# Kernel optimization log

Measured on AMD Instinct MI355X. Metric: run time of the kernel, lower is better.

Reference implementation:

```python
import jax, jax.numpy as jnp
import numpy as np

B, N, D = 64, 4096, 512
ATT = 128


def setup_inputs() -> dict:
    key = jax.random.key(0)
    ks = jax.random.split(key, 7)
    s = lambda fan_in: 1.0 / np.sqrt(fan_in)
    return {
        "v_I": jax.random.normal(ks[0], (B, N, D), dtype=jnp.float32),
        "v_Q": jax.random.normal(ks[1], (B, D), dtype=jnp.float32),
        "W_I": jax.random.normal(ks[2], (D, ATT), dtype=jnp.float32) * s(D),
        "W_Q": jax.random.normal(ks[3], (D, ATT), dtype=jnp.float32) * s(D),
        "b_Q": jnp.zeros((ATT,), dtype=jnp.float32),
        "W_p": jax.random.normal(ks[4], (ATT, 1), dtype=jnp.float32) * s(ATT),
        "b_p": jnp.zeros((1,), dtype=jnp.float32),
    }


def reference(v_I, v_Q, W_I, W_Q, b_Q, W_p, b_p):
    # v_I: [B, N, D], v_Q: [B, D]
    v_I_att = jnp.tanh(jnp.einsum("bnd,da->bna", v_I, W_I))          # [B, N, A]
    v_Q_att = jnp.tanh(v_Q @ W_Q + b_Q)[:, None, :]                  # [B, 1, A]
    h_A = jnp.tanh(v_I_att + v_Q_att)                                # [B, N, A]
    # dropout is identity in inference/reference mode
    p_I = (jnp.einsum("bna,ao->bno", h_A, W_p) + b_p)[..., 0]        # [B, N]
    p_I_output = jax.nn.softmax(p_I, axis=-1)                        # [B, N]
    v_att = jnp.einsum("bn,bnd->bd", p_I_output, v_I)                # [B, D]
    u = v_att + v_Q                                                  # [B, D]
    return (p_I_output, u)
```

## Files before the change

kernel.cpp:

```cpp
#include <hip/hip_runtime.h>
#include <cstdint>
#include <cstddef>

#define B_ 64
#define N_ 4096
#define D_ 512
#define A_ 128

typedef unsigned short u16;
typedef __attribute__((ext_vector_type(8))) short bf16x8;
typedef __attribute__((ext_vector_type(4))) float f32x4;

__device__ __forceinline__ u16 cvt_bf16(float x) {
    unsigned u = __float_as_uint(x);
    return (u16)((u + 0x7FFFu + ((u >> 16) & 1u)) >> 16);
}
__device__ __forceinline__ unsigned pack2_bf16(float a, float b) {
    unsigned ua = __float_as_uint(a), ub = __float_as_uint(b);
    unsigned ra = (ua + 0x7FFFu + ((ua >> 16) & 1u)) >> 16;
    unsigned rb = (ub + 0x7FFFu + ((ub >> 16) & 1u)) >> 16;
    return ra | (rb << 16);
}
__device__ __forceinline__ float bf2f(unsigned lo16) {
    return __uint_as_float(lo16 << 16);
}
__device__ __forceinline__ float fast_tanh(float x) {
    float ax = fabsf(x);
    float e  = __expf(-2.0f * ax);
    float r  = __fdividef(1.0f - e, 1.0f + e);
    return x < 0.0f ? -r : r;
}

#define WAITVM(N) asm volatile("s_waitcnt vmcnt(" #N ")" ::: "memory")
#define SCHEDB()  __builtin_amdgcn_sched_barrier(0)

__global__ void k_prep(const float* __restrict__ WI, const float* __restrict__ vQ,
                       const float* __restrict__ WQ, const float* __restrict__ bQ,
                       u16* __restrict__ Wbf, float* __restrict__ qatt,
                       float* __restrict__ sums, float* __restrict__ u_raw) {
    const int blk = blockIdx.x, t = threadIdx.x;
    if (blk < 64) {
        #pragma unroll
        for (int i = 0; i < 2; ++i) {
            int item = blk * 256 + i * 128 + t;
            int a  = item & 127;
            int d0 = (item >> 7) << 2;
            ushort4 r;
            r.x = cvt_bf16(WI[(d0 + 0) * A_ + a]);
            r.y = cvt_bf16(WI[(d0 + 1) * A_ + a]);
            r.z = cvt_bf16(WI[(d0 + 2) * A_ + a]);
            r.w = cvt_bf16(WI[(d0 + 3) * A_ + a]);
            int off = (a >> 4) * 8192
                    + (d0 >> 5) * 512
                    + ((d0 >> 3) & 3) * 128
                    + (a & 15) * 8
                    + (d0 & 7);
            *(ushort4*)&Wbf[off] = r;
        }
    } else {
        const int b = blk - 64;
        __shared__ float sq[D_];
        for (int d = t; d < D_; d += 128) sq[d] = vQ[b * D_ + d];
        __syncthreads();
        float acc = bQ[t];
        #pragma unroll 8
        for (int d = 0; d < D_; ++d) acc += sq[d] * WQ[d * A_ + t];
        qatt[b * A_ + t] = fast_tanh(acc);
        float4 z = {0.f, 0.f, 0.f, 0.f};
        *(float4*)(u_raw + b * D_ + t * 4) = z;
        if (t == 0) sums[b] = 0.0f;
    }
}

__global__ void __launch_bounds__(512, 4)
k_fused(const float* __restrict__ vI, const u16* __restrict__ Wbf,
        const float* __restrict__ qatt, const float* __restrict__ Wp,
        float* __restrict__ wbuf, float* __restrict__ sums,
        float* __restrict__ u_raw) {
    const int b  = blockIdx.y;
    const int n0 = blockIdx.x * 64;
    const int t    = threadIdx.x;
    const int lane = t & 63, wave = t >> 6;
    const int l15  = lane & 15, quad = lane >> 4;
    const int rg = wave >> 1, cg = wave & 1;

    __shared__ u16   sA[64 * 512];
    __shared__ float sred[2][64];
    __shared__ float sw[64];
    __shared__ float sph[4][512];

    float qa[4], wp[4];
    #pragma unroll
    for (int nt = 0; nt < 4; ++nt) {
        int a = (cg * 4 + nt) * 16 + l15;
        qa[nt] = qatt[b * A_ + a];
        wp[nt] = Wp[a];
    }
    SCHEDB();

    const int ar = t >> 3;
    const int ak = (t & 7) * 8;
    const float* ag = vI + ((size_t)(b * N_ + n0 + ar) * D_ + ak);
    char* awb = (char*)sA + ar * 1024 + (((t & 7) * 16) ^ ((ar & 7) << 4));

    const u16* bg = Wbf + lane * 8;

    const int arow = rg * 16 + l15;
    const char* afb = (const char*)sA + arow * 1024;
    const int aswz = (arow & 7) << 4;

    f32x4 acc[4];
    #pragma unroll
    for (int i = 0; i < 4; ++i) acc[i] = (f32x4){0.f, 0.f, 0.f, 0.f};

    float4 areg[2][2];
    areg[0][0] = *(const float4*)(ag + 0);
    areg[0][1] = *(const float4*)(ag + 4);
    SCHEDB();

    bf16x8 bf0[4], bf1[4];

    #pragma unroll
    for (int kr = 0; kr < 8; ++kr) {
        #pragma unroll
        for (int nt = 0; nt < 4; ++nt)
            bf0[nt] = *(const bf16x8*)(bg + ((((cg * 4 + nt) * 16) + kr * 2 + 0) << 9));
        SCHEDB();
        #pragma unroll
        for (int nt = 0; nt < 4; ++nt)
            bf1[nt] = *(const bf16x8*)(bg + ((((cg * 4 + nt) * 16) + kr * 2 + 1) << 9));
        SCHEDB();
        if (kr < 7) {
            areg[(kr + 1) & 1][0] = *(const float4*)(ag + (kr + 1) * 64);
            areg[(kr + 1) & 1][1] = *(const float4*)(ag + (kr + 1) * 64 + 4);
        }
        SCHEDB();

        if (kr < 7) { WAITVM(10); } else { WAITVM(8); }
        {
            float4 x0 = areg[kr & 1][0], x1 = areg[kr & 1][1];
            union { bf16x8 v; unsigned u[4]; } cv;
            cv.u[0] = pack2_bf16(x0.x, x0.y);
            cv.u[1] = pack2_bf16(x0.z, x0.w);
            cv.u[2] = pack2_bf16(x1.x, x1.y);
            cv.u[3] = pack2_bf16(x1.z, x1.w);
            *(bf16x8*)(awb + kr * 128) = cv.v;
        }
        SCHEDB();
        asm volatile("s_waitcnt lgkmcnt(0)" ::: "memory");
        __builtin_amdgcn_s_barrier();
        SCHEDB();

        if (kr < 7) { WAITVM(6); } else { WAITVM(4); }
        {
            bf16x8 af = *(const bf16x8*)(afb + kr * 128 + ((quad * 16) ^ aswz));
            #pragma unroll
            for (int nt = 0; nt < 4; ++nt)
                acc[nt] = __builtin_amdgcn_mfma_f32_16x16x32_bf16(af, bf0[nt], acc[nt], 0, 0, 0);
        }
        SCHEDB();
        if (kr < 7) { WAITVM(2); } else { WAITVM(0); }
        {
            bf16x8 af = *(const bf16x8*)(afb + kr * 128 + ((64 + quad * 16) ^ aswz));
            #pragma unroll
            for (int nt = 0; nt < 4; ++nt)
                acc[nt] = __builtin_amdgcn_mfma_f32_16x16x32_bf16(af, bf1[nt], acc[nt], 0, 0, 0);
        }
        SCHEDB();
    }

    #pragma unroll
    for (int r = 0; r < 4; ++r) {
        float s = 0.f;
        #pragma unroll
        for (int nt = 0; nt < 4; ++nt) {
            float t1 = fast_tanh(acc[nt][r]);
            float h  = fast_tanh(t1 + qa[nt]);
            s += h * wp[nt];
        }
        s += __shfl_xor(s, 1, 16);
        s += __shfl_xor(s, 2, 16);
        s += __shfl_xor(s, 4, 16);
        s += __shfl_xor(s, 8, 16);
        if (l15 == 0) sred[cg][rg * 16 + quad * 4 + r] = s;
    }
    __syncthreads();
    if (t < 64) {
        float we = __expf(sred[0][t] + sred[1][t]);
        sw[t] = we;
        wbuf[(size_t)b * N_ + n0 + t] = we;
        float ls = we;
        ls += __shfl_xor(ls, 1);
        ls += __shfl_xor(ls, 2);
        ls += __shfl_xor(ls, 4);
        ls += __shfl_xor(ls, 8);
        ls += __shfl_xor(ls, 16);
        ls += __shfl_xor(ls, 32);
        if (t == 0) atomicAdd(sums + b, ls);
    }
    __syncthreads();

    const int dg = t & 127;
    const int rr = t >> 7;
    float p0 = 0.f, p1 = 0.f, p2 = 0.f, p3 = 0.f;
    #pragma unroll
    for (int i = 0; i < 16; ++i) {
        int n = i * 4 + rr;
        const char* src = (const char*)sA + n * 1024 + ((dg * 8) ^ ((n & 7) << 4));
        uint2 wv = *(const uint2*)src;
        float wn = sw[n];
        p0 += wn * bf2f(wv.x & 0xffffu);
        p1 += wn * bf2f(wv.x >> 16);
        p2 += wn * bf2f(wv.y & 0xffffu);
        p3 += wn * bf2f(wv.y >> 16);
    }
    *(float4*)&sph[rr][dg * 4] = (float4){p0, p1, p2, p3};
    __syncthreads();
    {
        int d = t;
        float v = sph[0][d] + sph[1][d] + sph[2][d] + sph[3][d];
        atomicAdd(u_raw + (size_t)b * D_ + d, v);
    }
}

__global__ void __launch_bounds__(256)
k_fin(const float* __restrict__ wbuf, const float* __restrict__ sums,
      const float* __restrict__ u_raw, const float* __restrict__ vQ,
      float* __restrict__ p_out, float* __restrict__ u_out) {
    const int b = blockIdx.x, t = threadIdx.x;
    const float inv = 1.0f / sums[b];
    #pragma unroll
    for (int i = 0; i < 4; ++i) {
        float4 x = *(const float4*)(wbuf + (size_t)b * N_ + i * 1024 + t * 4);
        float4 y = { x.x * inv, x.y * inv, x.z * inv, x.w * inv };
        *(float4*)(p_out + (size_t)b * N_ + i * 1024 + t * 4) = y;
    }
    if (t < 128) {
        float4 ur = *(const float4*)(u_raw + b * D_ + t * 4);
        float4 vq = *(const float4*)(vQ + b * D_ + t * 4);
        float4 o  = { ur.x * inv + vq.x, ur.y * inv + vq.y,
                      ur.z * inv + vq.z, ur.w * inv + vq.w };
        *(float4*)(u_out + b * D_ + t * 4) = o;
    }
}

extern "C" void kernel_launch(void* const* d_in, const int* in_sizes, int n_in,
                              void* d_out, int out_size, void* d_ws, size_t ws_size,
                              hipStream_t stream) {
    const float* vI = (const float*)d_in[0];
    const float* vQ = (const float*)d_in[1];
    const float* WI = (const float*)d_in[2];
    const float* WQ = (const float*)d_in[3];
    const float* bQ = (const float*)d_in[4];
    const float* Wp = (const float*)d_in[5];

    float* out_p = (float*)d_out;
    float* out_u = out_p + (size_t)B_ * N_;

    char* ws = (char*)d_ws;
    u16*   Wbf   = (u16*)ws;
    float* qatt  = (float*)(ws + 131072);
    float* sums  = (float*)(ws + 163840);
    float* u_raw = (float*)(ws + 164864);
    float* wbuf  = (float*)(ws + 295936);

    k_prep<<<128, 128, 0, stream>>>(WI, vQ, WQ, bQ, Wbf, qatt, sums, u_raw);
    k_fused<<<dim3(N_ / 64, B_), 512, 0, stream>>>(vI, Wbf, qatt, Wp,
                                                   wbuf, sums, u_raw);
    k_fin<<<B_, 256, 0, stream>>>(wbuf, sums, u_raw, vQ, out_p, out_u);
}
```

Before: 762.6 us.

## Stage W_I tiles into LDS via global_load_lds shared across waves

Each wave previously loaded its own bf16 weight fragments straight from global memory into registers, so waves sharing a column group fetched the same data twice. Each wave now copies one 16-row slice of the weight tile into LDS per k-step with direct global-to-LDS loads, and all waves read B fragments from LDS. This adds a second barrier per iteration and raises LDS use to 80 KB, which may limit blocks per CU. The MFMA section also runs at raised wave priority, and the finalize kernel is split across four blocks per batch row to add parallelism.

```diff
diff --git a/kernel.cpp b/kernel.cpp
--- a/kernel.cpp
+++ b/kernel.cpp
@@ -29,6 +29,11 @@
     float e  = __expf(-2.0f * ax);
     float r  = __fdividef(1.0f - e, 1.0f + e);
     return x < 0.0f ? -r : r;
+}
+__device__ __forceinline__ void gl_lds16(const void* g, void* l) {
+    __builtin_amdgcn_global_load_lds(
+        (const __attribute__((address_space(1))) unsigned int*)g,
+        (__attribute__((address_space(3))) unsigned int*)l, 16, 0, 0);
 }
 
 #define WAITVM(N) asm volatile("s_waitcnt vmcnt(" #N ")" ::: "memory")
@@ -84,10 +89,12 @@
     const int l15  = lane & 15, quad = lane >> 4;
     const int rg = wave >> 1, cg = wave & 1;
 
-    __shared__ u16   sA[64 * 512];
-    __shared__ float sred[2][64];
-    __shared__ float sw[64];
-    __shared__ float sph[4][512];
+    __shared__ __align__(16) char smem[81920];
+    u16*  sA = (u16*)smem;
+    char* sB = smem + 65536;
+    float* sph  = (float*)sB;
+    float* sw   = (float*)(sB + 8192);
+    float* sred = (float*)(sB + 8448);
 
     float qa[4], wp[4];
     #pragma unroll
@@ -98,16 +105,18 @@
     }
     SCHEDB();
 
-    const int ar = t >> 3;
-    const int ak = (t & 7) * 8;
-    const float* ag = vI + ((size_t)(b * N_ + n0 + ar) * D_ + ak);
-    char* awb = (char*)sA + ar * 1024 + (((t & 7) * 16) ^ ((ar & 7) << 4));
-
-    const u16* bg = Wbf + lane * 8;
+    const int ar  = t >> 3;
+    const int akx = t & 7;
+    const float* ag = vI + ((size_t)(b * N_ + n0 + ar) * D_ + akx * 8);
+    char* awb = (char*)sA + ar * 1024 + ((akx * 16) ^ ((ar & 7) << 4));
+
+    const u16* bsrc = Wbf + (size_t)(wave * 16) * 512 + lane * 8;
+    char* bdst = sB + wave * 2048;
 
     const int arow = rg * 16 + l15;
     const char* afb = (const char*)sA + arow * 1024;
     const int aswz = (arow & 7) << 4;
+    const char* bfb = sB + (cg * 4) * 2048 + lane * 16;
 
     f32x4 acc[4];
     #pragma unroll
@@ -116,27 +125,20 @@
     float4 areg[2][2];
     areg[0][0] = *(const float4*)(ag + 0);
     areg[0][1] = *(const float4*)(ag + 4);
+    WAITVM(2);
     SCHEDB();
 
-    bf16x8 bf0[4], bf1[4];
-
     #pragma unroll
     for (int kr = 0; kr < 8; ++kr) {
-        #pragma unroll
-        for (int nt = 0; nt < 4; ++nt)
-            bf0[nt] = *(const bf16x8*)(bg + ((((cg * 4 + nt) * 16) + kr * 2 + 0) << 9));
-        SCHEDB();
-        #pragma unroll
-        for (int nt = 0; nt < 4; ++nt)
-            bf1[nt] = *(const bf16x8*)(bg + ((((cg * 4 + nt) * 16) + kr * 2 + 1) << 9));
+        gl_lds16(bsrc + (kr * 2 + 0) * 512, bdst);
+        gl_lds16(bsrc + (kr * 2 + 1) * 512, bdst + 1024);
         SCHEDB();
         if (kr < 7) {
             areg[(kr + 1) & 1][0] = *(const float4*)(ag + (kr + 1) * 64);
             areg[(kr + 1) & 1][1] = *(const float4*)(ag + (kr + 1) * 64 + 4);
         }
         SCHEDB();
-
-        if (kr < 7) { WAITVM(10); } else { WAITVM(8); }
+        if (kr < 7) { WAITVM(4); } else { WAITVM(2); }
         {
             float4 x0 = areg[kr & 1][0], x1 = areg[kr & 1][1];
             union { bf16x8 v; unsigned u[4]; } cv;
@@ -147,25 +149,23 @@
             *(bf16x8*)(awb + kr * 128) = cv.v;
         }
         SCHEDB();
+        if (kr < 7) { WAITVM(2); } else { WAITVM(0); }
         asm volatile("s_waitcnt lgkmcnt(0)" ::: "memory");
         __builtin_amdgcn_s_barrier();
         SCHEDB();
-
-        if (kr < 7) { WAITVM(6); } else { WAITVM(4); }
-        {
-            bf16x8 af = *(const bf16x8*)(afb + kr * 128 + ((quad * 16) ^ aswz));
+        __builtin_amdgcn_s_setprio(1);
+        #pragma unroll
+        for (int ks = 0; ks < 2; ++ks) {
+            bf16x8 af = *(const bf16x8*)(afb + kr * 128 + ((ks * 64 + quad * 16) ^ aswz));
             #pragma unroll
-            for (int nt = 0; nt < 4; ++nt)
-                acc[nt] = __builtin_amdgcn_mfma_f32_16x16x32_bf16(af, bf0[nt], acc[nt], 0, 0, 0);
-        }
-        SCHEDB();
-        if (kr < 7) { WAITVM(2); } else { WAITVM(0); }
-        {
-            bf16x8 af = *(const bf16x8*)(afb + kr * 128 + ((64 + quad * 16) ^ aswz));
-            #pragma unroll
-            for (int nt = 0; nt < 4; ++nt)
-                acc[nt] = __builtin_amdgcn_mfma_f32_16x16x32_bf16(af, bf1[nt], acc[nt], 0, 0, 0);
-        }
+            for (int nt = 0; nt < 4; ++nt) {
+                bf16x8 bv = *(const bf16x8*)(bfb + nt * 2048 + ks * 1024);
+                acc[nt] = __builtin_amdgcn_mfma_f32_16x16x32_bf16(af, bv, acc[nt], 0, 0, 0);
+            }
+        }
+        __builtin_amdgcn_s_setprio(0);
+        SCHEDB();
+        __builtin_amdgcn_s_barrier();
         SCHEDB();
     }
 
@@ -182,11 +182,11 @@
         s += __shfl_xor(s, 2, 16);
         s += __shfl_xor(s, 4, 16);
         s += __shfl_xor(s, 8, 16);
-        if (l15 == 0) sred[cg][rg * 16 + quad * 4 + r] = s;
+        if (l15 == 0) sred[cg * 64 + rg * 16 + quad * 4 + r] = s;
     }
     __syncthreads();
     if (t < 64) {
-        float we = __expf(sred[0][t] + sred[1][t]);
+        float we = __expf(sred[t] + sred[64 + t]);
         sw[t] = we;
         wbuf[(size_t)b * N_ + n0 + t] = we;
         float ls = we;
@@ -214,11 +214,11 @@
         p2 += wn * bf2f(wv.y & 0xffffu);
         p3 += wn * bf2f(wv.y >> 16);
     }
-    *(float4*)&sph[rr][dg * 4] = (float4){p0, p1, p2, p3};
+    *(float4*)(sph + rr * 512 + dg * 4) = (float4){p0, p1, p2, p3};
     __syncthreads();
     {
         int d = t;
-        float v = sph[0][d] + sph[1][d] + sph[2][d] + sph[3][d];
+        float v = sph[d] + sph[512 + d] + sph[1024 + d] + sph[1536 + d];
         atomicAdd(u_raw + (size_t)b * D_ + d, v);
     }
 }
@@ -227,15 +227,15 @@
 k_fin(const float* __restrict__ wbuf, const float* __restrict__ sums,
       const float* __restrict__ u_raw, const float* __restrict__ vQ,
       float* __restrict__ p_out, float* __restrict__ u_out) {
-    const int b = blockIdx.x, t = threadIdx.x;
+    const int b = blockIdx.x, q = blockIdx.y, t = threadIdx.x;
     const float inv = 1.0f / sums[b];
-    #pragma unroll
-    for (int i = 0; i < 4; ++i) {
-        float4 x = *(const float4*)(wbuf + (size_t)b * N_ + i * 1024 + t * 4);
+    {
+        size_t off = (size_t)b * N_ + q * 1024 + t * 4;
+        float4 x = *(const float4*)(wbuf + off);
         float4 y = { x.x * inv, x.y * inv, x.z * inv, x.w * inv };
-        *(float4*)(p_out + (size_t)b * N_ + i * 1024 + t * 4) = y;
-    }
-    if (t < 128) {
+        *(float4*)(p_out + off) = y;
+    }
+    if (q == 0 && t < 128) {
         float4 ur = *(const float4*)(u_raw + b * D_ + t * 4);
         float4 vq = *(const float4*)(vQ + b * D_ + t * 4);
         float4 o  = { ur.x * inv + vq.x, ur.y * inv + vq.y,
@@ -267,5 +267,5 @@
     k_prep<<<128, 128, 0, stream>>>(WI, vQ, WQ, bQ, Wbf, qatt, sums, u_raw);
     k_fused<<<dim3(N_ / 64, B_), 512, 0, stream>>>(vI, Wbf, qatt, Wp,
                                                    wbuf, sums, u_raw);
-    k_fin<<<B_, 256, 0, stream>>>(wbuf, sums, u_raw, vQ, out_p, out_u);
-}
+    k_fin<<<dim3(B_, 4), 256, 0, stream>>>(wbuf, sums, u_raw, vQ, out_p, out_u);
+}
```

Result: no change. 748.8 us (-1.8%).
